# Kernel tuning notes

Measured on AMD Instinct MI355X. Metric: run time of the kernel, lower is better.

The kernel has to match this reference:

```python
import jax, jax.numpy as jnp
from jax import lax
import numpy as np

DIM = 768
HEADS = 12
HD = DIM // HEADS  # 64
STRIDE = (1, 2, 2)
KER = (3, 3, 3)
PAD = [(1, 1), (1, 1), (1, 1)]
EPS = 1e-5


def _layernorm(x, g, b):
    mu = jnp.mean(x, axis=-1, keepdims=True)
    var = jnp.var(x, axis=-1, keepdims=True)
    return (x - mu) * lax.rsqrt(var + EPS) * g + b


def _attention_pool(t, wconv, g, b, T, H, W):
    # t: [B, heads, 1 + T*H*W, HD]; depthwise conv3d pooling on non-cls tokens
    B, Nh, _, Cd = t.shape
    cls_tok = t[:, :, :1, :]
    body = t[:, :, 1:, :].reshape(B * Nh, T, H, W, Cd).transpose(0, 4, 1, 2, 3)  # [BN, C, T, H, W]
    body = lax.conv_general_dilated(
        body, wconv, window_strides=STRIDE, padding=PAD,
        feature_group_count=Cd,
        dimension_numbers=('NCDHW', 'OIDHW', 'NCDHW'))
    Tp, Hp, Wp = body.shape[2], body.shape[3], body.shape[4]
    body = body.reshape(B, Nh, Cd, Tp * Hp * Wp).transpose(0, 1, 3, 2)  # [B, heads, Lp, C]
    t = jnp.concatenate([cls_tok, body], axis=2)
    t = _layernorm(t, g, b)
    return t, (Tp, Hp, Wp)


def setup_inputs() -> dict:
    key = jax.random.key(0)
    ks = jax.random.split(key, 12)
    T, H, W = 8, 28, 28
    B = 4
    N = 1 + T * H * W  # cls + thw tokens = 6273
    s = 0.02
    inp = {
        'x': jax.random.normal(ks[0], (B, N, DIM), jnp.float32),
        'qkv_w': jax.random.normal(ks[1], (DIM, 3 * DIM), jnp.float32) * s,
        'qkv_b': jnp.zeros((3 * DIM,), jnp.float32),
        'proj_w': jax.random.normal(ks[2], (DIM, DIM), jnp.float32) * s,
        'proj_b': jnp.zeros((DIM,), jnp.float32),
        'wq': jax.random.normal(ks[3], (HD, 1, 3, 3, 3), jnp.float32) * s,
        'wk': jax.random.normal(ks[4], (HD, 1, 3, 3, 3), jnp.float32) * s,
        'wv': jax.random.normal(ks[5], (HD, 1, 3, 3, 3), jnp.float32) * s,
        'gq': jnp.ones((HD,), jnp.float32), 'bq': jnp.zeros((HD,), jnp.float32),
        'gk': jnp.ones((HD,), jnp.float32), 'bk': jnp.zeros((HD,), jnp.float32),
        'gv': jnp.ones((HD,), jnp.float32), 'bv': jnp.zeros((HD,), jnp.float32),
        'thw_t': T, 'thw_h': H, 'thw_w': W,
    }
    return inp


def reference(x, qkv_w, qkv_b, proj_w, proj_b, wq, wk, wv,
              gq, bq, gk, bk, gv, bv, thw_t, thw_h, thw_w):
    B, N, C = x.shape
    scale = HD ** -0.5
    qkv = (x @ qkv_w + qkv_b).reshape(B, N, 3, HEADS, HD).transpose(2, 0, 3, 1, 4)
    q, k, v = qkv[0], qkv[1], qkv[2]  # [B, heads, N, HD]
    q, q_shape = _attention_pool(q, wq, gq, bq, thw_t, thw_h, thw_w)
    k, _ = _attention_pool(k, wk, gk, bk, thw_t, thw_h, thw_w)
    v, _ = _attention_pool(v, wv, gv, bv, thw_t, thw_h, thw_w)
    attn = jax.nn.softmax(jnp.einsum('bhqd,bhkd->bhqk', q, k) * scale, axis=-1)
    Nq = q.shape[2]
    out = jnp.einsum('bhqk,bhkd->bhqd', attn, v).transpose(0, 2, 1, 3).reshape(B, Nq, C)
    out = out @ proj_w + proj_b
    return out
```

## Files before the change

kernel.cpp:

```cpp
#include <hip/hip_runtime.h>
#include <hip/hip_bf16.h>

#define BB      4
#define NTOK    6273
#define NPOOL   1569
#define NPOOLP  1600
#define NHEADS  12
#define TT      8
#define HH      28
#define WW      28
#define HP      14
#define WP      14

typedef __attribute__((ext_vector_type(8))) _Float16 f16x8;
typedef __attribute__((ext_vector_type(4))) float f32x4;
typedef unsigned short u16;

#define AS1(p) ((const __attribute__((address_space(1))) void*)(p))
#define AS3(p) ((__attribute__((address_space(3))) void*)(p))

static __device__ __forceinline__ u16 f2h(float x) {
    union { _Float16 h; u16 u; } c; c.h = (_Float16)x; return c.u;
}
static __device__ __forceinline__ float h2f(u16 u) {
    union { u16 u; _Float16 h; } c; c.u = u; return (float)c.h;
}

__global__ __launch_bounds__(256) void cvt_f32_f16_kernel(
    const float* __restrict__ in, u16* __restrict__ out, int n4)
{
    int i = blockIdx.x * 256 + threadIdx.x;
    const int stride = gridDim.x * 256;
    for (; i < n4; i += stride) {
        const float4 v = ((const float4*)in)[i];
        ushort4 o;
        o.x = f2h(v.x); o.y = f2h(v.y); o.z = f2h(v.z); o.w = f2h(v.w);
        ((ushort4*)out)[i] = o;
    }
}

__global__ __launch_bounds__(256) void transpose_cvt_kernel(
    const float* __restrict__ W, u16* __restrict__ t, int K, int N)
{
    __shared__ float tile[32][33];
    const int n0 = blockIdx.x * 32, k0 = blockIdx.y * 32;
    const int tx = threadIdx.x, ty = threadIdx.y;
    #pragma unroll
    for (int i = 0; i < 4; ++i)
        tile[ty + i * 8][tx] = W[(size_t)(k0 + ty + i * 8) * N + n0 + tx];
    __syncthreads();
    #pragma unroll
    for (int i = 0; i < 4; ++i) {
        const int n = n0 + ty + i * 8;
        t[(size_t)n * K + k0 + tx] = f2h(tile[tx][ty + i * 8]);
    }
}

__global__ __launch_bounds__(256) void wt_transpose_kernel(
    const float* __restrict__ wq, const float* __restrict__ wk,
    const float* __restrict__ wv, u16* __restrict__ wTh)
{
    const int which = blockIdx.x;
    const float* w = (which == 0) ? wq : (which == 1) ? wk : wv;
    u16* o = wTh + which * 27 * 64;
    for (int i = threadIdx.x; i < 27 * 64; i += 256) {
        const int j = i >> 6, d = i & 63;
        o[j * 64 + d] = f2h(w[d * 27 + j]);
    }
}

template<int NBLK, bool QKV, typename OutT>
__global__ __launch_bounds__(512) void gemm_fp16_kernel(
    const u16* __restrict__ Af, const u16* __restrict__ Bt,
    const float* __restrict__ bias, int M,
    OutT* __restrict__ o0, OutT* __restrict__ o1, OutT* __restrict__ o2)
{
    __shared__ __align__(16) u16 A_s[128 * 32];
    __shared__ __align__(16) u16 B_s[128 * 32];

    const int tid  = threadIdx.x;
    const int lane = tid & 63;
    const int w    = tid >> 6;
    const int wr   = w >> 2, wc = w & 3;

    const int nwg = gridDim.x;
    const int qch = nwg >> 3, rch = nwg & 7;
    const int xcd = blockIdx.x & 7, idx = blockIdx.x >> 3;
    const int wg  = (xcd < rch ? xcd * (qch + 1) : rch * (qch + 1) + (xcd - rch) * qch) + idx;
    const int m0 = (wg / NBLK) * 128;
    const int n0 = (wg % NBLK) * 128;

    f32x4 acc[4][2] = {};

    const int srow   = lane >> 2;
    const int sslot  = (lane & 3) ^ ((srow >> 1) & 3);

    for (int kt = 0; kt < 24; ++kt) {
        const int k0 = kt * 32;
        __syncthreads();

        {
            const int rb = w * 16;
            const int ra = min(m0 + rb + srow, M - 1);
            __builtin_amdgcn_global_load_lds(AS1(Af + (size_t)ra * 768 + k0 + sslot * 8),
                                             AS3(&A_s[rb * 32]), 16, 0, 0);
            __builtin_amdgcn_global_load_lds(AS1(Bt + (size_t)(n0 + rb + srow) * 768 + k0 + sslot * 8),
                                             AS3(&B_s[rb * 32]), 16, 0, 0);
        }
        __syncthreads();

        const int fr = lane & 15, fq = lane >> 4;
        const int rslot = (fq ^ ((fr >> 1) & 3)) << 3;
        f16x8 a[4], b[2];
        #pragma unroll
        for (int m = 0; m < 4; ++m)
            a[m] = *(const f16x8*)&A_s[(wr * 64 + m * 16 + fr) * 32 + rslot];
        #pragma unroll
        for (int n = 0; n < 2; ++n)
            b[n] = *(const f16x8*)&B_s[(wc * 32 + n * 16 + fr) * 32 + rslot];

        #pragma unroll
        for (int m = 0; m < 4; ++m)
            #pragma unroll
            for (int n = 0; n < 2; ++n)
                acc[m][n] = __builtin_amdgcn_mfma_f32_16x16x32_f16(a[m], b[n], acc[m][n], 0, 0, 0);
    }

    const int fr = lane & 15, fq = lane >> 4;
    #pragma unroll
    for (int m = 0; m < 4; ++m) {
        const int grow_base = m0 + wr * 64 + m * 16 + fq * 4;
        #pragma unroll
        for (int j = 0; j < 4; ++j) {
            const int grow = grow_base + j;
            if (grow >= M) continue;
            int b = 0, ntok = 0;
            if (QKV) { b = grow / NTOK; ntok = grow - b * NTOK; }
            #pragma unroll
            for (int n = 0; n < 2; ++n) {
                const int gcol = n0 + wc * 32 + n * 16 + fr;
                const float v = acc[m][n][j] + bias[gcol];
                if (QKV) {
                    const int s = gcol / 768;
                    const int rem = gcol - s * 768;
                    const int h = rem >> 6, d = rem & 63;
                    OutT* dst = (s == 0) ? o0 : (s == 1) ? o1 : o2;
                    dst[(size_t)((b * NHEADS + h) * NTOK + ntok) * 64 + d] = (OutT)f2h(v);
                } else {
                    o0[(size_t)grow * (NBLK * 128) + gcol] = (OutT)v;
                }
            }
        }
    }
}

#define PL_PG  50
#define PL_NWG (3 * 48 * PL_PG)
__global__ __launch_bounds__(256) void pool_ln_kernel(
    const u16* __restrict__ qr, const u16* __restrict__ kr, const u16* __restrict__ vr,
    const u16* __restrict__ wTh,
    const float* __restrict__ gq, const float* __restrict__ bq,
    const float* __restrict__ gk, const float* __restrict__ bk,
    const float* __restrict__ gv, const float* __restrict__ bv,
    u16* __restrict__ qph, u16* __restrict__ kph, u16* __restrict__ vpt)
{
    const int wg = (blockIdx.x & 7) * (PL_NWG / 8) + (blockIdx.x >> 3);
    const int which = wg / (48 * PL_PG);
    const int rem   = wg - which * (48 * PL_PG);
    const int bh    = rem / PL_PG;
    const int pg    = rem - bh * PL_PG;
    const int wv_   = threadIdx.x >> 6;
    const int lane  = threadIdx.x & 63;
    const int tg    = lane >> 3;
    const int d0    = (lane & 7) * 8;

    const int p  = pg * 32 + wv_ * 8 + tg;
    const int pc = min(p, NPOOL - 1);

    const u16*   in  = (which == 0) ? qr : (which == 1) ? kr : vr;
    const u16*   wTb = wTh + which * 27 * 64;
    const float* g   = (which == 0) ? gq : (which == 1) ? gk : gv;
    const float* bb_ = (which == 0) ? bq : (which == 1) ? bk : bv;
    const float qscale = (which == 0) ? 0.125f : 1.0f;

    const size_t inb = (size_t)bh * NTOK * 64;

    float s[8] = {};
    if (pc == 0) {
        const f16x8 t = *(const f16x8*)&in[inb + d0];
        #pragma unroll
        for (int c = 0; c < 8; ++c) s[c] = (float)t[c];
    } else {
        const int idx = pc - 1;
        const int tp = idx / (HP * WP);
        const int r2 = idx - tp * (HP * WP);
        const int hp = r2 / WP;
        const int wp = r2 - hp * WP;

        const f16x8 z8 = (f16x8)(_Float16)0.0f;
        #pragma unroll
        for (int kt = 0; kt < 3; ++kt) {
            const int it = tp + kt - 1;
            #pragma unroll
            for (int kh = 0; kh < 3; ++kh) {
                const int ih = hp * 2 + kh - 1;
                #pragma unroll
                for (int kw = 0; kw < 3; ++kw) {
                    const int iw = wp * 2 + kw - 1;
                    const int j  = kt * 9 + kh * 3 + kw;
                    const bool ok = (it >= 0) & (it < TT) & (ih >= 0) & (ih < HH) &
                                    (iw >= 0) & (iw < WW);
                    const int n   = 1 + (it * HH + ih) * WW + iw;
                    const int n_c = ok ? n : 0;
                    const f16x8 tv  = *(const f16x8*)&in[inb + (size_t)n_c * 64 + d0];
                    const f16x8 wv8 = *(const f16x8*)&wTb[j * 64 + d0];
                    const f16x8 ts  = ok ? tv : z8;
                    #pragma unroll
                    for (int c = 0; c < 8; ++c)
                        s[c] = fmaf((float)wv8[c], (float)ts[c], s[c]);
                }
            }
        }
    }

    float sum = 0.f, ssq = 0.f;
    #pragma unroll
    for (int c = 0; c < 8; ++c) { sum += s[c]; ssq += s[c] * s[c]; }
    #pragma unroll
    for (int off = 1; off < 8; off <<= 1) {
        sum += __shfl_xor(sum, off);
        ssq += __shfl_xor(ssq, off);
    }
    const float mu  = sum * (1.f / 64.f);
    const float var = ssq * (1.f / 64.f) - mu * mu;
    const float rs  = rsqrtf(var + 1e-5f);

    float g8[8], b8[8];
    {
        const float4 g0 = *(const float4*)&g[d0];
        const float4 g1 = *(const float4*)&g[d0 + 4];
        const float4 b0 = *(const float4*)&bb_[d0];
        const float4 b1 = *(const float4*)&bb_[d0 + 4];
        g8[0]=g0.x; g8[1]=g0.y; g8[2]=g0.z; g8[3]=g0.w;
        g8[4]=g1.x; g8[5]=g1.y; g8[6]=g1.z; g8[7]=g1.w;
        b8[0]=b0.x; b8[1]=b0.y; b8[2]=b0.z; b8[3]=b0.w;
        b8[4]=b1.x; b8[5]=b1.y; b8[6]=b1.z; b8[7]=b1.w;
    }

    u16 oo[8];
    #pragma unroll
    for (int c = 0; c < 8; ++c)
        oo[c] = f2h(((s[c] - mu) * rs * g8[c] + b8[c]) * qscale);

    if (which == 2) {
        u16* base = vpt + (size_t)bh * 64 * NPOOLP + p;
        if (p < NPOOL) {
            #pragma unroll
            for (int c = 0; c < 8; ++c)
                base[(size_t)(d0 + c) * NPOOLP] = oo[c];
        } else {
            #pragma unroll
            for (int c = 0; c < 8; ++c)
                base[(size_t)(d0 + c) * NPOOLP] = 0;
        }
    } else if (p < NPOOL) {
        u16* out = (which == 0) ? qph : kph;
        u16* dst = &out[((size_t)bh * NPOOL + p) * 64 + d0];
        *(ushort4*)&dst[0] = *(ushort4*)&oo[0];
        *(ushort4*)&dst[4] = *(ushort4*)&oo[4];
    }
}

__global__ __launch_bounds__(256) void flash_attn_fp16_kernel(
    const u16* __restrict__ qh, const u16* __restrict__ kh,
    const u16* __restrict__ vt, float* __restrict__ accf,
    float* __restrict__ lf)
{
    __shared__ __align__(16) u16 K_s[64 * 64];
    __shared__ __align__(16) u16 V_s[64 * 64];
    __shared__ __align__(16) u16 P_s[4][32 * 64];

    const int bh = blockIdx.y;
    const int q0 = blockIdx.x * 128;
    const int z  = blockIdx.z;
    const int kt_lo = z ? 13 : 0, kt_hi = z ? 25 : 13;
    const int tid = threadIdx.x;
    const int w = tid >> 6, lane = tid & 63;
    const int fr = lane & 15, fq = lane >> 4;
    const int l8 = lane >> 3;
    const int sw = 8 * ((lane & 7) ^ l8);

    const size_t hb  = (size_t)bh * NPOOL * 64;
    const size_t vtb = (size_t)bh * 64 * NPOOLP;
    float* accb = accf + (size_t)z * BB * NPOOL * 768;
    float* lb   = lf   + (size_t)z * 48 * NPOOL;

    f16x8 qf_[2][2];
    #pragma unroll
    for (int qf = 0; qf < 2; ++qf) {
        const int row = min(q0 + w * 32 + qf * 16 + fr, NPOOL - 1);
        #pragma unroll
        for (int half = 0; half < 2; ++half)
            qf_[qf][half] = *(const f16x8*)&qh[hb + (size_t)row * 64 + half * 32 + fq * 8];
    }

    f16x8 ones;
    #pragma unroll
    for (int i = 0; i < 8; ++i) ones[i] = (_Float16)1.0f;

    f32x4 acc[2][4] = {};
    f32x4 l_acc[2] = {};

    #define LDSW(buf, row, colbyte) \
        (*(const f16x8*)((const char*)(buf) + ((row) * 128 + ((colbyte) ^ (((row) & 7) << 4)))))

    for (int kt = kt_lo; kt < kt_hi; ++kt) {
        const int k0 = kt * 64;
        __syncthreads();

        #pragma unroll
        for (int i = 0; i < 2; ++i) {
            const int rb = w * 16 + i * 8;
            const int r  = rb + l8;
            const int gk = min(k0 + r, NPOOL - 1);
            __builtin_amdgcn_global_load_lds(AS1(kh + hb + (size_t)gk * 64 + sw),
                                             AS3(&K_s[rb * 64]), 16, 0, 0);
            __builtin_amdgcn_global_load_lds(AS1(vt + vtb + (size_t)r * NPOOLP + k0 + sw),
                                             AS3(&V_s[rb * 64]), 16, 0, 0);
        }
        __syncthreads();

        f32x4 sv[2][4];
        #pragma unroll
        for (int nf = 0; nf < 4; ++nf) {
            const int krow = nf * 16 + fr;
            const f16x8 kf0 = LDSW(K_s, krow, fq * 16);
            const f16x8 kf1 = LDSW(K_s, krow, 64 + fq * 16);
            #pragma unroll
            for (int qf = 0; qf < 2; ++qf) {
                f32x4 s = {};
                s = __builtin_amdgcn_mfma_f32_16x16x32_f16(qf_[qf][0], kf0, s, 0, 0, 0);
                s = __builtin_amdgcn_mfma_f32_16x16x32_f16(qf_[qf][1], kf1, s, 0, 0, 0);
                sv[qf][nf] = s;
            }
        }

        #pragma unroll
        for (int nf = 0; nf < 4; ++nf) {
            const bool valid = (k0 + nf * 16 + fr) < NPOOL;
            #pragma unroll
            for (int qf = 0; qf < 2; ++qf) {
                #pragma unroll
                for (int j = 0; j < 4; ++j) {
                    const float p = valid ? __expf(sv[qf][nf][j]) : 0.f;
                    const int row = qf * 16 + fq * 4 + j;
                    const int bo  = row * 128 + ((nf * 32 + fr * 2) ^ ((row & 7) << 4));
                    *(u16*)((char*)&P_s[w][0] + bo) = f2h(p);
                }
            }
        }
        __builtin_amdgcn_sched_barrier(0);

        f16x8 pa[2][2];
        #pragma unroll
        for (int qf = 0; qf < 2; ++qf) {
            const int prow = qf * 16 + fr;
            pa[qf][0] = LDSW(&P_s[w][0], prow, fq * 16);
            pa[qf][1] = LDSW(&P_s[w][0], prow, 64 + fq * 16);
            l_acc[qf] = __builtin_amdgcn_mfma_f32_16x16x32_f16(pa[qf][0], ones, l_acc[qf], 0, 0, 0);
            l_acc[qf] = __builtin_amdgcn_mfma_f32_16x16x32_f16(pa[qf][1], ones, l_acc[qf], 0, 0, 0);
        }
        #pragma unroll
        for (int df = 0; df < 4; ++df) {
            const int vrow = df * 16 + fr;
            const f16x8 v0 = LDSW(V_s, vrow, fq * 16);
            const f16x8 v1 = LDSW(V_s, vrow, 64 + fq * 16);
            acc[0][df] = __builtin_amdgcn_mfma_f32_16x16x32_f16(pa[0][0], v0, acc[0][df], 0, 0, 0);
            acc[0][df] = __builtin_amdgcn_mfma_f32_16x16x32_f16(pa[0][1], v1, acc[0][df], 0, 0, 0);
            acc[1][df] = __builtin_amdgcn_mfma_f32_16x16x32_f16(pa[1][0], v0, acc[1][df], 0, 0, 0);
            acc[1][df] = __builtin_amdgcn_mfma_f32_16x16x32_f16(pa[1][1], v1, acc[1][df], 0, 0, 0);
        }
    }
    #undef LDSW

    const int b = bh / NHEADS, h = bh % NHEADS;
    #pragma unroll
    for (int qf = 0; qf < 2; ++qf) {
        #pragma unroll
        for (int j = 0; j < 4; ++j) {
            const int q = q0 + w * 32 + qf * 16 + fq * 4 + j;
            if (q >= NPOOL) continue;
            float* dst = &accb[((size_t)b * NPOOL + q) * 768 + h * 64];
            #pragma unroll
            for (int df = 0; df < 4; ++df)
                dst[df * 16 + fr] = acc[qf][df][j];
            if (fr == 0)
                lb[(size_t)bh * NPOOL + q] = l_acc[qf][j];
        }
    }
}

__global__ __launch_bounds__(256) void combine_kernel(
    const float* __restrict__ acc0, const float* __restrict__ acc1,
    const float* __restrict__ l0, const float* __restrict__ l1,
    u16* __restrict__ aoh)
{
    const int n4 = BB * NPOOL * 768 / 4;
    int i = blockIdx.x * 256 + threadIdx.x;
    const int stride = gridDim.x * 256;
    for (; i < n4; i += stride) {
        const int e0  = i * 4;
        const int row = e0 / 768;
        const int c   = e0 - row * 768;
        const int b   = row / NPOOL;
        const int q   = row - b * NPOOL;
        const int h   = c >> 6;
        const size_t li = (size_t)(b * NHEADS + h) * NPOOL + q;
        const float inv = 1.f / (l0[li] + l1[li]);
        const float4 a0 = ((const float4*)acc0)[i];
        const float4 a1 = ((const float4*)acc1)[i];
        ushort4 o;
        o.x = f2h((a0.x + a1.x) * inv);
        o.y = f2h((a0.y + a1.y) * inv);
        o.z = f2h((a0.z + a1.z) * inv);
        o.w = f2h((a0.w + a1.w) * inv);
        ((ushort4*)aoh)[i] = o;
    }
}

extern "C" void kernel_launch(void* const* d_in, const int* in_sizes, int n_in,
                              void* d_out, int out_size, void* d_ws, size_t ws_size,
                              hipStream_t stream)
{
    const float* x      = (const float*)d_in[0];
    const float* qkv_w  = (const float*)d_in[1];
    const float* qkv_b  = (const float*)d_in[2];
    const float* proj_w = (const float*)d_in[3];
    const float* proj_b = (const float*)d_in[4];
    const float* wq     = (const float*)d_in[5];
    const float* wk     = (const float*)d_in[6];
    const float* wv     = (const float*)d_in[7];
    const float* gq     = (const float*)d_in[8];
    const float* bq     = (const float*)d_in[9];
    const float* gk     = (const float*)d_in[10];
    const float* bk     = (const float*)d_in[11];
    const float* gv     = (const float*)d_in[12];
    const float* bv     = (const float*)d_in[13];

    const size_t RAW  = (size_t)BB * NHEADS * NTOK * 64;
    const size_t PLD  = (size_t)BB * NHEADS * NPOOL * 64;
    const size_t VTSZ = (size_t)BB * NHEADS * 64 * NPOOLP;
    const size_t AOSZ = (size_t)BB * NPOOL * 768;

    u16* q_raw = (u16*)d_ws;
    u16* k_raw = q_raw + RAW;
    u16* v_raw = k_raw + RAW;
    u16* xh    = v_raw + RAW;
    u16* qph   = xh + RAW;
    u16* kph   = qph + PLD;
    u16* vpb   = kph + PLD;
    u16* vpt   = vpb + PLD;
    u16* wth   = vpt + VTSZ;
    u16* pwth  = wth + (size_t)2304 * 768;
    u16* wTh   = pwth + (size_t)768 * 768;
    float* acc0 = (float*)(wTh + 3 * 27 * 64);
    float* acc1 = acc0 + AOSZ;
    float* l0   = acc1 + AOSZ;
    float* l1   = l0 + (size_t)48 * NPOOL;
    u16* aoh   = q_raw;

    cvt_f32_f16_kernel<<<2048, 256, 0, stream>>>(x, xh, (int)(RAW / 4));

    transpose_cvt_kernel<<<dim3(2304 / 32, 768 / 32), dim3(32, 8), 0, stream>>>(
        qkv_w, wth, 768, 2304);
    transpose_cvt_kernel<<<dim3(768 / 32, 768 / 32), dim3(32, 8), 0, stream>>>(
        proj_w, pwth, 768, 768);
    wt_transpose_kernel<<<3, 256, 0, stream>>>(wq, wk, wv, wTh);

    gemm_fp16_kernel<18, true, u16><<<dim3(197 * 18), 512, 0, stream>>>(
        xh, wth, qkv_b, BB * NTOK, q_raw, k_raw, v_raw);

    pool_ln_kernel<<<dim3(PL_NWG), 256, 0, stream>>>(
        q_raw, k_raw, v_raw, wTh, gq, bq, gk, bk, gv, bv,
        qph, kph, vpt);

    flash_attn_fp16_kernel<<<dim3(13, 48, 2), 256, 0, stream>>>(
        qph, kph, vpt, acc0, l0);

    combine_kernel<<<2048, 256, 0, stream>>>(acc0, acc1, l0, l1, aoh);

    gemm_fp16_kernel<6, false, float><<<dim3(50 * 6), 512, 0, stream>>>(
        aoh, pwth, proj_b, BB * NPOOL, (float*)d_out, nullptr, nullptr);
}
```

Measured before the change: 343.3 us.

## Replace QKV GEMM with 256x256-tile triple-buffered fp16 MFMA kernel

Adds a new QKV projection GEMM that uses 256x256 output tiles instead of 128x128, with a three-stage LDS buffer filled through global_load_lds and split A/B staging interleaved with the MFMA work. The goal is more data reuse per loaded tile and better hiding of global load latency in the largest GEMM. In exchange it uses far more LDS and accumulator registers per workgroup, which may limit occupancy. It also leaves a partially filled last M tile, which wastes compute.

```diff
diff --git a/kernel.cpp b/kernel.cpp
--- a/kernel.cpp
+++ b/kernel.cpp
@@ -66,6 +66,123 @@
     for (int i = threadIdx.x; i < 27 * 64; i += 256) {
         const int j = i >> 6, d = i & 63;
         o[j * 64 + d] = f2h(w[d * 27 + j]);
+    }
+}
+
+#define GBK 32
+#define GNKT 24
+
+__global__ __launch_bounds__(512, 2) void gemm256_qkv_kernel(
+    const u16* __restrict__ Af, const u16* __restrict__ Bt,
+    const float* __restrict__ bias, int M,
+    u16* __restrict__ o0, u16* __restrict__ o1, u16* __restrict__ o2)
+{
+    __shared__ __align__(16) u16 AB_s[3][2][256 * GBK];
+
+    const int tid  = threadIdx.x;
+    const int lane = tid & 63;
+    const int w    = tid >> 6;
+    const int wr   = w >> 2, wc = w & 3;
+
+    const int nwg = gridDim.x;
+    const int qch = nwg >> 3, rch = nwg & 7;
+    const int xcd = blockIdx.x & 7, idx = blockIdx.x >> 3;
+    const int wg  = (xcd < rch ? xcd * (qch + 1) : rch * (qch + 1) + (xcd - rch) * qch) + idx;
+    const int m0 = (wg / 9) * 256;
+    const int nb = wg % 9;
+    const int n0 = nb * 256;
+
+    const int ch0 = tid, ch1 = 512 + tid;
+    const int r0 = ch0 >> 2, c0 = ((ch0 & 3) ^ (r0 & 3)) << 3;
+    const int r1 = ch1 >> 2, c1 = ((ch1 & 3) ^ (r1 & 3)) << 3;
+    const u16* pA0 = Af + (size_t)min(m0 + r0, M - 1) * 768 + c0;
+    const u16* pA1 = Af + (size_t)min(m0 + r1, M - 1) * 768 + c1;
+    const u16* pB0 = Bt + (size_t)(n0 + r0) * 768 + c0;
+    const u16* pB1 = Bt + (size_t)(n0 + r1) * 768 + c1;
+    const int dst0 = (w * 64) * 8;
+    const int dst1 = (512 + w * 64) * 8;
+
+    #define STAGE_A(buf, kk) do { \
+        __builtin_amdgcn_global_load_lds(AS1(pA0 + (kk)), AS3(&AB_s[buf][0][dst0]), 16, 0, 0); \
+        __builtin_amdgcn_global_load_lds(AS1(pA1 + (kk)), AS3(&AB_s[buf][0][dst1]), 16, 0, 0); \
+    } while (0)
+    #define STAGE_B(buf, kk) do { \
+        __builtin_amdgcn_global_load_lds(AS1(pB0 + (kk)), AS3(&AB_s[buf][1][dst0]), 16, 0, 0); \
+        __builtin_amdgcn_global_load_lds(AS1(pB1 + (kk)), AS3(&AB_s[buf][1][dst1]), 16, 0, 0); \
+    } while (0)
+
+    STAGE_A(0, 0);  STAGE_B(0, 0);
+    STAGE_A(1, GBK); STAGE_B(1, GBK);
+
+    f32x4 acc[8][4] = {};
+    const int fr = lane & 15, fq = lane >> 4;
+    const int sw8 = (fq ^ (fr & 3)) << 3;
+
+    int bufc = 0;
+    for (int t = 0; t < GNKT; ++t) {
+        if (t < GNKT - 1) asm volatile("s_waitcnt vmcnt(4)" ::: "memory");
+        else              asm volatile("s_waitcnt vmcnt(0)" ::: "memory");
+        __builtin_amdgcn_s_barrier();
+
+        const u16* As = &AB_s[bufc][0][0];
+        const u16* Bs = &AB_s[bufc][1][0];
+        const int bufs = (bufc + 2 >= 3) ? bufc - 1 : bufc + 2;
+        const int kk = (t + 2) * GBK;
+
+        if (t < GNKT - 2) STAGE_A(bufs, kk);
+        f16x8 a[4], b[4];
+        #pragma unroll
+        for (int m = 0; m < 4; ++m)
+            a[m] = *(const f16x8*)&As[(wr * 128 + m * 16 + fr) * GBK + sw8];
+        #pragma unroll
+        for (int n = 0; n < 4; ++n)
+            b[n] = *(const f16x8*)&Bs[(wc * 64 + n * 16 + fr) * GBK + sw8];
+        __builtin_amdgcn_s_setprio(1);
+        #pragma unroll
+        for (int m = 0; m < 4; ++m)
+            #pragma unroll
+            for (int n = 0; n < 4; ++n)
+                acc[m][n] = __builtin_amdgcn_mfma_f32_16x16x32_f16(a[m], b[n], acc[m][n], 0, 0, 0);
+        __builtin_amdgcn_s_setprio(0);
+        __builtin_amdgcn_s_barrier();
+
+        if (t < GNKT - 2) STAGE_B(bufs, kk);
+        #pragma unroll
+        for (int m = 0; m < 4; ++m)
+            a[m] = *(const f16x8*)&As[(wr * 128 + (m + 4) * 16 + fr) * GBK + sw8];
+        __builtin_amdgcn_s_setprio(1);
+        #pragma unroll
+        for (int m = 0; m < 4; ++m)
+            #pragma unroll
+            for (int n = 0; n < 4; ++n)
+                acc[m + 4][n] = __builtin_amdgcn_mfma_f32_16x16x32_f16(a[m], b[n], acc[m + 4][n], 0, 0, 0);
+        __builtin_amdgcn_s_setprio(0);
+
+        bufc = (bufc + 1 >= 3) ? 0 : bufc + 1;
+    }
+    #undef STAGE_A
+    #undef STAGE_B
+
+    const int s = nb / 3;
+    u16* const dsts = (s == 0) ? o0 : (s == 1) ? o1 : o2;
+    #pragma unroll
+    for (int m = 0; m < 8; ++m) {
+        const int growb = m0 + wr * 128 + m * 16 + fq * 4;
+        #pragma unroll
+        for (int j = 0; j < 4; ++j) {
+            const int grow = growb + j;
+            if (grow >= M) continue;
+            const int bidx = grow / NTOK;
+            const int ntok = grow - bidx * NTOK;
+            #pragma unroll
+            for (int n = 0; n < 4; ++n) {
+                const int gcol = n0 + wc * 64 + n * 16 + fr;
+                const float v = acc[m][n][j] + bias[gcol];
+                const int rem = gcol - s * 768;
+                const int h = rem >> 6, d = rem & 63;
+                dsts[(size_t)((bidx * NHEADS + h) * NTOK + ntok) * 64 + d] = f2h(v);
+            }
+        }
     }
 }
 
@@ -477,7 +594,7 @@
         proj_w, pwth, 768, 768);
     wt_transpose_kernel<<<3, 256, 0, stream>>>(wq, wk, wv, wTh);
 
-    gemm_fp16_kernel<18, true, u16><<<dim3(197 * 18), 512, 0, stream>>>(
+    gemm256_qkv_kernel<<<dim3(99 * 9), 512, 0, stream>>>(
         xh, wth, qkv_b, BB * NTOK, q_raw, k_raw, v_raw);
 
     pool_ln_kernel<<<dim3(PL_NWG), 256, 0, stream>>>(
```

New measurement: 324.6 us. 5.5% less time.

## Replace QKV GEMM with 256x128 tile double-buffered LDS kernel

Applied to the files above, without the earlier changes.

Adds a dedicated QKV projection GEMM that uses 256x128 output tiles with double-buffered LDS staging through direct global-to-LDS loads, and launches it in place of the generic 128-tile kernel. Larger M tiles give more reuse of each B tile, and prefetching the next K slice is meant to overlap loads with MFMA work. The cost is more LDS and registers per workgroup (64 accumulators per lane), which may lower occupancy, plus some wasted rows in the last M tile.

```diff
diff --git a/kernel.cpp b/kernel.cpp
--- a/kernel.cpp
+++ b/kernel.cpp
@@ -66,6 +66,107 @@
     for (int i = threadIdx.x; i < 27 * 64; i += 256) {
         const int j = i >> 6, d = i & 63;
         o[j * 64 + d] = f2h(w[d * 27 + j]);
+    }
+}
+
+#define GBK 32
+#define GNKT 24
+
+__global__ __launch_bounds__(512, 4) void gemm256_qkv_kernel(
+    const u16* __restrict__ Af, const u16* __restrict__ Bt,
+    const float* __restrict__ bias, int M,
+    u16* __restrict__ o0, u16* __restrict__ o1, u16* __restrict__ o2)
+{
+    __shared__ __align__(16) u16 A_s[2][256 * GBK];
+    __shared__ __align__(16) u16 B_s[2][128 * GBK];
+
+    const int tid  = threadIdx.x;
+    const int lane = tid & 63;
+    const int w    = tid >> 6;
+    const int wr   = w >> 1, wc = w & 1;
+
+    const int nwg = gridDim.x;
+    const int qch = nwg >> 3, rch = nwg & 7;
+    const int xcd = blockIdx.x & 7, idx = blockIdx.x >> 3;
+    const int wg  = (xcd < rch ? xcd * (qch + 1) : rch * (qch + 1) + (xcd - rch) * qch) + idx;
+    const int m0 = (wg / 18) * 256;
+    const int nb = wg % 18;
+    const int n0 = nb * 128;
+
+    const int rA0 = tid >> 2;
+    const int cA0 = ((tid & 3) ^ ((rA0 >> 1) & 3)) << 3;
+    const int ch1 = 512 + tid;
+    const int rA1 = ch1 >> 2;
+    const int cA1 = ((ch1 & 3) ^ ((rA1 >> 1) & 3)) << 3;
+    const u16* pA0 = Af + (size_t)min(m0 + rA0, M - 1) * 768 + cA0;
+    const u16* pA1 = Af + (size_t)min(m0 + rA1, M - 1) * 768 + cA1;
+    const u16* pB  = Bt + (size_t)(n0 + rA0) * 768 + cA0;
+    const int dstA0 = (w * 64) * 8;
+    const int dstA1 = (512 + w * 64) * 8;
+    const int dstB  = (w * 64) * 8;
+
+    #define STAGE(buf, kk) do { \
+        __builtin_amdgcn_global_load_lds(AS1(pA0 + (kk)), AS3(&A_s[buf][dstA0]), 16, 0, 0); \
+        __builtin_amdgcn_global_load_lds(AS1(pA1 + (kk)), AS3(&A_s[buf][dstA1]), 16, 0, 0); \
+        __builtin_amdgcn_global_load_lds(AS1(pB  + (kk)), AS3(&B_s[buf][dstB ]), 16, 0, 0); \
+    } while (0)
+
+    STAGE(0, 0);
+
+    f32x4 acc[4][4] = {};
+    const int fr = lane & 15, fq = lane >> 4;
+    const int sw8 = (fq ^ ((fr >> 1) & 3)) << 3;
+
+    for (int t = 0; t < GNKT; ++t) {
+        const int cur = t & 1;
+        if (t < GNKT - 1) {
+            STAGE(cur ^ 1, (t + 1) * GBK);
+            asm volatile("s_waitcnt vmcnt(3)" ::: "memory");
+        } else {
+            asm volatile("s_waitcnt vmcnt(0)" ::: "memory");
+        }
+        __builtin_amdgcn_s_barrier();
+
+        f16x8 a[4], b[4];
+        #pragma unroll
+        for (int m = 0; m < 4; ++m)
+            a[m] = *(const f16x8*)&A_s[cur][(wr * 64 + m * 16 + fr) * GBK + sw8];
+        #pragma unroll
+        for (int n = 0; n < 4; ++n)
+            b[n] = *(const f16x8*)&B_s[cur][(wc * 64 + n * 16 + fr) * GBK + sw8];
+
+        __builtin_amdgcn_s_setprio(1);
+        #pragma unroll
+        for (int m = 0; m < 4; ++m)
+            #pragma unroll
+            for (int n = 0; n < 4; ++n)
+                acc[m][n] = __builtin_amdgcn_mfma_f32_16x16x32_f16(a[m], b[n], acc[m][n], 0, 0, 0);
+        __builtin_amdgcn_s_setprio(0);
+
+        if (t < GNKT - 1) __builtin_amdgcn_s_barrier();
+    }
+    #undef STAGE
+
+    const int s = nb / 6;
+    u16* const dsts = (s == 0) ? o0 : (s == 1) ? o1 : o2;
+    #pragma unroll
+    for (int m = 0; m < 4; ++m) {
+        const int growb = m0 + wr * 64 + m * 16 + fq * 4;
+        #pragma unroll
+        for (int j = 0; j < 4; ++j) {
+            const int grow = growb + j;
+            if (grow >= M) continue;
+            const int bidx = grow / NTOK;
+            const int ntok = grow - bidx * NTOK;
+            #pragma unroll
+            for (int n = 0; n < 4; ++n) {
+                const int gcol = n0 + wc * 64 + n * 16 + fr;
+                const float v = acc[m][n][j] + bias[gcol];
+                const int rem = gcol - s * 768;
+                const int h = rem >> 6, d = rem & 63;
+                dsts[(size_t)((bidx * NHEADS + h) * NTOK + ntok) * 64 + d] = f2h(v);
+            }
+        }
     }
 }
 
@@ -477,7 +578,7 @@
         proj_w, pwth, 768, 768);
     wt_transpose_kernel<<<3, 256, 0, stream>>>(wq, wk, wv, wTh);
 
-    gemm_fp16_kernel<18, true, u16><<<dim3(197 * 18), 512, 0, stream>>>(
+    gemm256_qkv_kernel<<<dim3(99 * 18), 512, 0, stream>>>(
         xh, wth, qkv_b, BB * NTOK, q_raw, k_raw, v_raw);
 
     pool_ln_kernel<<<dim3(PL_NWG), 256, 0, stream>>>(
```

Result: faster. 307.0 us (-10.6%).
